# Performance work log

Measured on AMD Instinct MI355X. Metric: run time of the kernel, lower is better.

Reference implementation:

```python
import jax, jax.numpy as jnp
import numpy as np

B, S, F, H = 64, 1024, 128, 512  # batch, seq_len, features, lstm units


def setup_inputs() -> dict:
    key = jax.random.key(0)
    k1, k2, k3 = jax.random.split(key, 3)
    x = jax.random.normal(k1, (B, S, F), dtype=jnp.float32)
    # Keras LSTM params: kernel [F, 4H], recurrent_kernel [H, 4H], bias [4H]
    W = jax.random.normal(k2, (F, 4 * H), dtype=jnp.float32) * (1.0 / np.sqrt(F))
    U = jax.random.normal(k3, (H, 4 * H), dtype=jnp.float32) * (1.0 / np.sqrt(H))
    b = jnp.zeros((4 * H,), dtype=jnp.float32)
    return {"x": x, "W": W, "U": U, "b": b}


def _lstm_relu(x, W, U, b):
    # Precompute input projection for all timesteps: [B,S,4H]
    xW = jnp.einsum("bsf,fg->bsg", x, W) + b
    xW_t = jnp.transpose(xW, (1, 0, 2))  # [S,B,4H] for scan over time
    h0 = jnp.zeros((x.shape[0], H), dtype=x.dtype)
    c0 = jnp.zeros((x.shape[0], H), dtype=x.dtype)

    def step(carry, xw):
        h, c = carry
        z = xw + h @ U  # [B,4H]
        zi, zf, zg, zo = jnp.split(z, 4, axis=-1)  # Keras gate order i,f,c,o
        i = jax.nn.sigmoid(zi)
        f = jax.nn.sigmoid(zf)
        g = jax.nn.relu(zg)          # activation='relu' (candidate)
        o = jax.nn.sigmoid(zo)
        c_new = f * c + i * g
        h_new = o * jax.nn.relu(c_new)  # activation='relu' (output)
        return (h_new, c_new), h_new

    _, hs = jax.lax.scan(step, (h0, c0), xW_t)
    return jnp.transpose(hs, (1, 0, 2))  # [B,S,H]


def reference(x, W, U, b):
    # LSTM(return_sequences=True, activation='relu'); Dropout inactive at inference.
    return _lstm_relu(x, W, U, b)
```

## Files before the change

### kernel.cpp

```cpp
#include <hip/hip_runtime.h>
#include <stdint.h>


#define S_ 1024
#define F_ 128
#define H_ 512
#define G4_ 2048
#define SLOTS 32
#define KH 16
#define LDKS 640
#define HB (64 * H_)

typedef __attribute__((ext_vector_type(8))) short short8;
typedef __attribute__((ext_vector_type(4))) float f32x4;
typedef unsigned long long ull;

__device__ __forceinline__ unsigned short f2bf(float f) {
  union { float f; unsigned u; } v; v.f = f;
  unsigned u = v.u + 0x7fffu + ((v.u >> 16) & 1u);
  return (unsigned short)(u >> 16);
}

__device__ __forceinline__ short8 pack2(f32x4 a, f32x4 b) {
  short8 r;
#pragma unroll
  for (int i = 0; i < 4; ++i) r[i] = (short)f2bf(a[i]);
#pragma unroll
  for (int i = 0; i < 4; ++i) r[4 + i] = (short)f2bf(b[i]);
  return r;
}

__device__ __forceinline__ int swz(int cc, int k) {
  return (cc * LDKS + k) ^ ((cc & 7) << 3);
}

__global__ __launch_bounds__(256, 1) void lstm_pers(
    const float* __restrict__ x, const float* __restrict__ W,
    const float* __restrict__ U, const float* __restrict__ bias,
    float* __restrict__ out, unsigned int* ws_sync, unsigned short* hbuf) {

  __shared__ unsigned short V[64 * LDKS];
  __shared__ f32x4 R[2][4][4][64];
  __shared__ int meta[2];

  const int tid  = threadIdx.x;
  const int w    = tid >> 6;
  const int lane = tid & 63;
  const int l15  = lane & 15;
  const int l4   = lane >> 4;
  const int koff = l4 * 8;

  if (tid == 0) {
    unsigned int xcc;
    asm volatile("s_getreg_b32 %0, hwreg(20, 0, 4)" : "=s"(xcc));
    xcc &= 7;
    unsigned sv = atomicAdd(ws_sync + xcc * 32, 1u);
    meta[0] = (int)xcc;
    meta[1] = (int)(sv & 31);
  }
  __syncthreads();
  const int xcc  = meta[0];
  const int slot = meta[1];

  unsigned int* gflags = ws_sync + 256 + xcc * 128;
  unsigned int* myflag = gflags + slot * 4 + w;
  unsigned int* pollp  = gflags + 32 * w + (lane & 31);

  const int u0    = slot * 16;
  const int bbase = xcc * 8;

  for (int idx = tid; idx < (64 * LDKS) / 4; idx += 256) {
    const int q4   = idx & 15;
    const int k    = idx >> 4;
    const int gate = q4 & 3;
    const int ul0  = (q4 >> 2) * 4;
    const int col  = gate * H_ + u0 + ul0;
    const float* src = (k < H_) ? (U + (size_t)k * G4_ + col)
                                : (W + (size_t)(k - H_) * G4_ + col);
    const f32x4 v4 = *(const f32x4*)src;
#pragma unroll
    for (int q = 0; q < 4; ++q) {
      const int ul = ul0 + q;
      const int cc = (ul >> 2) * 16 + (ul & 3) * 4 + gate;
      V[swz(cc, k)] = f2bf(v4[q]);
    }
  }

  float bias_r[4];
#pragma unroll
  for (int g = 0; g < 4; ++g) bias_r[g] = bias[g * H_ + u0 + w * 4 + l4];

  __syncthreads();

  const int brow = bbase + (l15 & 7);
  const float* xrow = x + (size_t)brow * S_ * F_ + koff + w * 32;
  const unsigned short* hrow0 = hbuf + (size_t)brow * H_ + koff;
  const int myunit = u0 + w * 4 + l4;

  float cst = 0.f;

  f32x4 xa = *(const f32x4*)(xrow);
  f32x4 xb = *(const f32x4*)(xrow + 4);

  for (int t = 0; t < S_; ++t) {
    f32x4 acc[4];
#pragma unroll
    for (int tl = 0; tl < 4; ++tl) { acc[tl][0]=0.f; acc[tl][1]=0.f; acc[tl][2]=0.f; acc[tl][3]=0.f; }
    {
      const short8 bx = pack2(xa, xb);
      const int k0 = (KH + w) * 32 + koff;
#pragma unroll
      for (int tl = 0; tl < 4; ++tl) {
        const short8 a = *(const short8*)&V[swz(tl * 16 + l15, k0)];
        acc[tl] = __builtin_amdgcn_mfma_f32_16x16x32_bf16(a, bx, acc[tl], 0, 0, 0);
      }
    }

    {
      const int tn = (t + 1 < S_) ? t + 1 : t;
      const float* xt = xrow + (size_t)tn * F_;
      xa = *(const f32x4*)(xt);
      xb = *(const f32x4*)(xt + 4);
    }

    if (t > 0) {
      const unsigned tgt = (unsigned)t;
      while (true) {
        unsigned v = __hip_atomic_load(pollp, __ATOMIC_RELAXED, __HIP_MEMORY_SCOPE_AGENT);
        if (__all((int)(v >= tgt))) break;
      }
      asm volatile("" ::: "memory");

      const unsigned short* hr = hrow0 + (size_t)(t & 1) * HB;
      short8 bh[4];
#pragma unroll
      for (int i = 0; i < 4; ++i) {
        union { ull u[2]; short8 s; } bb;
        const ull* hq = (const ull*)(hr + (4 * w + i) * 32);
        bb.u[0] = __hip_atomic_load(hq,     __ATOMIC_RELAXED, __HIP_MEMORY_SCOPE_AGENT);
        bb.u[1] = __hip_atomic_load(hq + 1, __ATOMIC_RELAXED, __HIP_MEMORY_SCOPE_AGENT);
        bh[i] = bb.s;
      }
#pragma unroll
      for (int i = 0; i < 4; ++i) {
        const int k0 = (4 * w + i) * 32 + koff;
#pragma unroll
        for (int tl = 0; tl < 4; ++tl) {
          const short8 a = *(const short8*)&V[swz(tl * 16 + l15, k0)];
          acc[tl] = __builtin_amdgcn_mfma_f32_16x16x32_bf16(a, bh[i], acc[tl], 0, 0, 0);
        }
      }
    }

    const int p = t & 1;
#pragma unroll
    for (int tl = 0; tl < 4; ++tl) R[p][w][tl][lane] = acc[tl];
    __syncthreads();

    f32x4 z;
    {
      const f32x4 r0 = R[p][0][w][lane], r1 = R[p][1][w][lane],
                  r2 = R[p][2][w][lane], r3 = R[p][3][w][lane];
#pragma unroll
      for (int g = 0; g < 4; ++g)
        z[g] = bias_r[g] + r0[g] + r1[g] + r2[g] + r3[g];
    }

    const float ig = 1.f / (1.f + __expf(-z[0]));
    const float fg = 1.f / (1.f + __expf(-z[1]));
    const float gg = fmaxf(z[2], 0.f);
    const float og = 1.f / (1.f + __expf(-z[3]));
    const float cn = fg * cst + ig * gg;
    cst = cn;
    const float hv = og * fmaxf(cn, 0.f);

    if (l15 < 8)
      hbuf[(size_t)((t + 1) & 1) * HB + (size_t)brow * H_ + myunit] = f2bf(hv);
    asm volatile("s_waitcnt vmcnt(0)" ::: "memory");
    if (lane == 0)
      __hip_atomic_store(myflag, (unsigned)(t + 1), __ATOMIC_RELAXED, __HIP_MEMORY_SCOPE_AGENT);
    if (l15 < 8)
      out[((size_t)brow * S_ + t) * H_ + myunit] = hv;
  }
}

extern "C" void kernel_launch(void* const* d_in, const int* in_sizes, int n_in,
                              void* d_out, int out_size, void* d_ws, size_t ws_size,
                              hipStream_t stream) {
  const float* x = (const float*)d_in[0];
  const float* W = (const float*)d_in[1];
  const float* U = (const float*)d_in[2];
  const float* b = (const float*)d_in[3];
  float* out = (float*)d_out;

  unsigned int*   ws_sync = (unsigned int*)d_ws;
  unsigned short* hbuf    = (unsigned short*)((char*)d_ws + 32768);

  hipMemsetAsync(d_ws, 0, 32768, stream);

  lstm_pers<<<dim3(256), dim3(256), 0, stream>>>(x, W, U, b, out, ws_sync, hbuf);
}
```

Measured before the change: 2.732 ms.

## Give each wave its own unit rows and drop the per-step cross-wave reduction

Result: slower. 8.160 ms (+198.7%).

```diff
diff --git a/kernel.cpp b/kernel.cpp
--- a/kernel.cpp
+++ b/kernel.cpp
@@ -6,7 +6,6 @@
 #define F_ 128
 #define H_ 512
 #define G4_ 2048
-#define SLOTS 32
 #define KH 16
 #define LDKS 640
 #define HB (64 * H_)
@@ -40,8 +39,8 @@
     float* __restrict__ out, unsigned int* ws_sync, unsigned short* hbuf) {
 
   __shared__ unsigned short V[64 * LDKS];
-  __shared__ f32x4 R[2][4][4][64];
   __shared__ int meta[2];
+  __shared__ unsigned join_ctr;
 
   const int tid  = threadIdx.x;
   const int w    = tid >> 6;
@@ -57,14 +56,13 @@
     unsigned sv = atomicAdd(ws_sync + xcc * 32, 1u);
     meta[0] = (int)xcc;
     meta[1] = (int)(sv & 31);
+    join_ctr = 0u;
   }
   __syncthreads();
   const int xcc  = meta[0];
   const int slot = meta[1];
 
-  unsigned int* gflags = ws_sync + 256 + xcc * 128;
-  unsigned int* myflag = gflags + slot * 4 + w;
-  unsigned int* pollp  = gflags + 32 * w + (lane & 31);
+  unsigned int* gline = ws_sync + 256 + xcc * 32;
 
   const int u0    = slot * 16;
   const int bbase = xcc * 8;
@@ -93,78 +91,73 @@
   __syncthreads();
 
   const int brow = bbase + (l15 & 7);
-  const float* xrow = x + (size_t)brow * S_ * F_ + koff + w * 32;
+  const float* xrow = x + (size_t)brow * S_ * F_ + koff;
   const unsigned short* hrow0 = hbuf + (size_t)brow * H_ + koff;
   const int myunit = u0 + w * 4 + l4;
+  const int vrow   = w * 16 + l15;
 
   float cst = 0.f;
 
-  f32x4 xa = *(const f32x4*)(xrow);
-  f32x4 xb = *(const f32x4*)(xrow + 4);
+  f32x4 xa[4], xb[4];
+#pragma unroll
+  for (int q = 0; q < 4; ++q) {
+    xa[q] = *(const f32x4*)(xrow + q * 32);
+    xb[q] = *(const f32x4*)(xrow + q * 32 + 4);
+  }
 
   for (int t = 0; t < S_; ++t) {
     f32x4 acc[4];
 #pragma unroll
-    for (int tl = 0; tl < 4; ++tl) { acc[tl][0]=0.f; acc[tl][1]=0.f; acc[tl][2]=0.f; acc[tl][3]=0.f; }
-    {
-      const short8 bx = pack2(xa, xb);
-      const int k0 = (KH + w) * 32 + koff;
-#pragma unroll
-      for (int tl = 0; tl < 4; ++tl) {
-        const short8 a = *(const short8*)&V[swz(tl * 16 + l15, k0)];
-        acc[tl] = __builtin_amdgcn_mfma_f32_16x16x32_bf16(a, bx, acc[tl], 0, 0, 0);
-      }
+    for (int q = 0; q < 4; ++q) { acc[q][0]=0.f; acc[q][1]=0.f; acc[q][2]=0.f; acc[q][3]=0.f; }
+
+#pragma unroll
+    for (int q = 0; q < 4; ++q) {
+      const short8 bx = pack2(xa[q], xb[q]);
+      const short8 a  = *(const short8*)&V[swz(vrow, (KH + q) * 32 + koff)];
+      acc[q] = __builtin_amdgcn_mfma_f32_16x16x32_bf16(a, bx, acc[q], 0, 0, 0);
     }
 
     {
       const int tn = (t + 1 < S_) ? t + 1 : t;
       const float* xt = xrow + (size_t)tn * F_;
-      xa = *(const f32x4*)(xt);
-      xb = *(const f32x4*)(xt + 4);
+#pragma unroll
+      for (int q = 0; q < 4; ++q) {
+        xa[q] = *(const f32x4*)(xt + q * 32);
+        xb[q] = *(const f32x4*)(xt + q * 32 + 4);
+      }
     }
 
     if (t > 0) {
       const unsigned tgt = (unsigned)t;
-      while (true) {
-        unsigned v = __hip_atomic_load(pollp, __ATOMIC_RELAXED, __HIP_MEMORY_SCOPE_AGENT);
-        if (__all((int)(v >= tgt))) break;
-      }
-      asm volatile("" ::: "memory");
-
       const unsigned short* hr = hrow0 + (size_t)(t & 1) * HB;
-      short8 bh[4];
-#pragma unroll
-      for (int i = 0; i < 4; ++i) {
-        union { ull u[2]; short8 s; } bb;
-        const ull* hq = (const ull*)(hr + (4 * w + i) * 32);
-        bb.u[0] = __hip_atomic_load(hq,     __ATOMIC_RELAXED, __HIP_MEMORY_SCOPE_AGENT);
-        bb.u[1] = __hip_atomic_load(hq + 1, __ATOMIC_RELAXED, __HIP_MEMORY_SCOPE_AGENT);
-        bh[i] = bb.s;
-      }
-#pragma unroll
-      for (int i = 0; i < 4; ++i) {
-        const int k0 = (4 * w + i) * 32 + koff;
-#pragma unroll
-        for (int tl = 0; tl < 4; ++tl) {
-          const short8 a = *(const short8*)&V[swz(tl * 16 + l15, k0)];
-          acc[tl] = __builtin_amdgcn_mfma_f32_16x16x32_bf16(a, bh[i], acc[tl], 0, 0, 0);
+#pragma unroll
+      for (int ci = 0; ci < 4; ++ci) {
+        const int c = (w + ci) & 3;
+        while (true) {
+          const unsigned fl = __hip_atomic_load(gline + (lane & 31),
+                                                __ATOMIC_RELAXED, __HIP_MEMORY_SCOPE_AGENT);
+          ull m = __ballot((int)(fl >= tgt));
+          m &= (m >> 32);
+          if (((m >> (8 * c)) & 0xFFull) == 0xFFull) break;
+        }
+        asm volatile("" ::: "memory");
+#pragma unroll
+        for (int i = 0; i < 4; ++i) {
+          const int ks = 4 * c + i;
+          union { ull u[2]; short8 s; } bb;
+          const ull* hq = (const ull*)(hr + ks * 32);
+          bb.u[0] = __hip_atomic_load(hq,     __ATOMIC_RELAXED, __HIP_MEMORY_SCOPE_AGENT);
+          bb.u[1] = __hip_atomic_load(hq + 1, __ATOMIC_RELAXED, __HIP_MEMORY_SCOPE_AGENT);
+          const short8 a = *(const short8*)&V[swz(vrow, ks * 32 + koff)];
+          acc[ci] = __builtin_amdgcn_mfma_f32_16x16x32_bf16(a, bb.s, acc[ci], 0, 0, 0);
         }
       }
     }
 
-    const int p = t & 1;
-#pragma unroll
-    for (int tl = 0; tl < 4; ++tl) R[p][w][tl][lane] = acc[tl];
-    __syncthreads();
-
     f32x4 z;
-    {
-      const f32x4 r0 = R[p][0][w][lane], r1 = R[p][1][w][lane],
-                  r2 = R[p][2][w][lane], r3 = R[p][3][w][lane];
-#pragma unroll
-      for (int g = 0; g < 4; ++g)
-        z[g] = bias_r[g] + r0[g] + r1[g] + r2[g] + r3[g];
-    }
+#pragma unroll
+    for (int g = 0; g < 4; ++g)
+      z[g] = bias_r[g] + acc[0][g] + acc[1][g] + acc[2][g] + acc[3][g];
 
     const float ig = 1.f / (1.f + __expf(-z[0]));
     const float fg = 1.f / (1.f + __expf(-z[1]));
@@ -177,8 +170,14 @@
     if (l15 < 8)
       hbuf[(size_t)((t + 1) & 1) * HB + (size_t)brow * H_ + myunit] = f2bf(hv);
     asm volatile("s_waitcnt vmcnt(0)" ::: "memory");
-    if (lane == 0)
-      __hip_atomic_store(myflag, (unsigned)(t + 1), __ATOMIC_RELAXED, __HIP_MEMORY_SCOPE_AGENT);
+
+    if (lane == 0) {
+      const unsigned old = atomicAdd(&join_ctr, 1u);
+      if (old == 4u * (unsigned)t + 3u)
+        __hip_atomic_store(gline + slot, (unsigned)(t + 1),
+                           __ATOMIC_RELAXED, __HIP_MEMORY_SCOPE_AGENT);
+    }
+
     if (l15 < 8)
       out[((size_t)brow * S_ + t) * H_ + myunit] = hv;
   }
```

## Embed parity flags in h sign bits and replace swizzle with LDS padding

Applied to the files above, without the earlier changes.

After: 2.716 ms. Within noise of the previous version (-0.6%).

```diff
diff --git a/kernel.cpp b/kernel.cpp
--- a/kernel.cpp
+++ b/kernel.cpp
@@ -6,10 +6,12 @@
 #define F_ 128
 #define H_ 512
 #define G4_ 2048
-#define SLOTS 32
 #define KH 16
-#define LDKS 640
+#define KDIM 640
+#define LDKS 648
 #define HB (64 * H_)
+#define SMASK 0x8000800080008000ull
+#define VMASK 0x7FFF7FFF7FFF7FFFull
 
 typedef __attribute__((ext_vector_type(8))) short short8;
 typedef __attribute__((ext_vector_type(4))) float f32x4;
@@ -28,10 +30,6 @@
 #pragma unroll
   for (int i = 0; i < 4; ++i) r[4 + i] = (short)f2bf(b[i]);
   return r;
-}
-
-__device__ __forceinline__ int swz(int cc, int k) {
-  return (cc * LDKS + k) ^ ((cc & 7) << 3);
 }
 
 __global__ __launch_bounds__(256, 1) void lstm_pers(
@@ -62,14 +60,14 @@
   const int xcc  = meta[0];
   const int slot = meta[1];
 
-  unsigned int* gflags = ws_sync + 256 + xcc * 128;
-  unsigned int* myflag = gflags + slot * 4 + w;
-  unsigned int* pollp  = gflags + 32 * w + (lane & 31);
+  unsigned int* eline = ws_sync + 256 + xcc * 32;
+  unsigned int* myep  = eline + slot;
+  unsigned int* epp   = eline + (lane & 31);
 
   const int u0    = slot * 16;
   const int bbase = xcc * 8;
 
-  for (int idx = tid; idx < (64 * LDKS) / 4; idx += 256) {
+  for (int idx = tid; idx < (64 * KDIM) / 4; idx += 256) {
     const int q4   = idx & 15;
     const int k    = idx >> 4;
     const int gate = q4 & 3;
@@ -82,7 +80,7 @@
     for (int q = 0; q < 4; ++q) {
       const int ul = ul0 + q;
       const int cc = (ul >> 2) * 16 + (ul & 3) * 4 + gate;
-      V[swz(cc, k)] = f2bf(v4[q]);
+      V[cc * LDKS + k] = f2bf(v4[q]);
     }
   }
 
@@ -103,6 +101,10 @@
   f32x4 xb = *(const f32x4*)(xrow + 4);
 
   for (int t = 0; t < S_; ++t) {
+    unsigned ev = 0xFFFFFFFFu;
+    if (w == 0 && t >= 2)
+      ev = __hip_atomic_load(epp, __ATOMIC_RELAXED, __HIP_MEMORY_SCOPE_AGENT);
+
     f32x4 acc[4];
 #pragma unroll
     for (int tl = 0; tl < 4; ++tl) { acc[tl][0]=0.f; acc[tl][1]=0.f; acc[tl][2]=0.f; acc[tl][3]=0.f; }
@@ -111,7 +113,7 @@
       const int k0 = (KH + w) * 32 + koff;
 #pragma unroll
       for (int tl = 0; tl < 4; ++tl) {
-        const short8 a = *(const short8*)&V[swz(tl * 16 + l15, k0)];
+        const short8 a = *(const short8*)&V[(tl * 16 + l15) * LDKS + k0];
         acc[tl] = __builtin_amdgcn_mfma_f32_16x16x32_bf16(a, bx, acc[tl], 0, 0, 0);
       }
     }
@@ -124,29 +126,40 @@
     }
 
     if (t > 0) {
-      const unsigned tgt = (unsigned)t;
+      const ull expm = (((((t - 1) >> 1) & 1) ^ 1) ? SMASK : 0ull);
+      const unsigned short* hr = hrow0 + (size_t)(t & 1) * HB;
+      const ull* q0 = (const ull*)(hr + (4 * w + 0) * 32);
+      const ull* q1 = (const ull*)(hr + (4 * w + 1) * 32);
+      const ull* q2 = (const ull*)(hr + (4 * w + 2) * 32);
+      const ull* q3 = (const ull*)(hr + (4 * w + 3) * 32);
+      ull v0, v1, v2, v3, v4, v5, v6, v7;
       while (true) {
-        unsigned v = __hip_atomic_load(pollp, __ATOMIC_RELAXED, __HIP_MEMORY_SCOPE_AGENT);
-        if (__all((int)(v >= tgt))) break;
+        v0 = __hip_atomic_load(q0,     __ATOMIC_RELAXED, __HIP_MEMORY_SCOPE_AGENT);
+        v1 = __hip_atomic_load(q0 + 1, __ATOMIC_RELAXED, __HIP_MEMORY_SCOPE_AGENT);
+        v2 = __hip_atomic_load(q1,     __ATOMIC_RELAXED, __HIP_MEMORY_SCOPE_AGENT);
+        v3 = __hip_atomic_load(q1 + 1, __ATOMIC_RELAXED, __HIP_MEMORY_SCOPE_AGENT);
+        v4 = __hip_atomic_load(q2,     __ATOMIC_RELAXED, __HIP_MEMORY_SCOPE_AGENT);
+        v5 = __hip_atomic_load(q2 + 1, __ATOMIC_RELAXED, __HIP_MEMORY_SCOPE_AGENT);
+        v6 = __hip_atomic_load(q3,     __ATOMIC_RELAXED, __HIP_MEMORY_SCOPE_AGENT);
+        v7 = __hip_atomic_load(q3 + 1, __ATOMIC_RELAXED, __HIP_MEMORY_SCOPE_AGENT);
+        const bool ok = ((v0 & SMASK) == expm) & ((v1 & SMASK) == expm) &
+                        ((v2 & SMASK) == expm) & ((v3 & SMASK) == expm) &
+                        ((v4 & SMASK) == expm) & ((v5 & SMASK) == expm) &
+                        ((v6 & SMASK) == expm) & ((v7 & SMASK) == expm);
+        if (__all((int)ok)) break;
       }
-      asm volatile("" ::: "memory");
-
-      const unsigned short* hr = hrow0 + (size_t)(t & 1) * HB;
-      short8 bh[4];
-#pragma unroll
-      for (int i = 0; i < 4; ++i) {
-        union { ull u[2]; short8 s; } bb;
-        const ull* hq = (const ull*)(hr + (4 * w + i) * 32);
-        bb.u[0] = __hip_atomic_load(hq,     __ATOMIC_RELAXED, __HIP_MEMORY_SCOPE_AGENT);
-        bb.u[1] = __hip_atomic_load(hq + 1, __ATOMIC_RELAXED, __HIP_MEMORY_SCOPE_AGENT);
-        bh[i] = bb.s;
-      }
+      union { ull u[2]; short8 s; } b0, b1, b2, b3;
+      b0.u[0] = v0 & VMASK; b0.u[1] = v1 & VMASK;
+      b1.u[0] = v2 & VMASK; b1.u[1] = v3 & VMASK;
+      b2.u[0] = v4 & VMASK; b2.u[1] = v5 & VMASK;
+      b3.u[0] = v6 & VMASK; b3.u[1] = v7 & VMASK;
+      const short8 bh[4] = {b0.s, b1.s, b2.s, b3.s};
 #pragma unroll
       for (int i = 0; i < 4; ++i) {
         const int k0 = (4 * w + i) * 32 + koff;
 #pragma unroll
         for (int tl = 0; tl < 4; ++tl) {
-          const short8 a = *(const short8*)&V[swz(tl * 16 + l15, k0)];
+          const short8 a = *(const short8*)&V[(tl * 16 + l15) * LDKS + k0];
           acc[tl] = __builtin_amdgcn_mfma_f32_16x16x32_bf16(a, bh[i], acc[tl], 0, 0, 0);
         }
       }
@@ -155,7 +168,16 @@
     const int p = t & 1;
 #pragma unroll
     for (int tl = 0; tl < 4; ++tl) R[p][w][tl][lane] = acc[tl];
+
+    if (w == 0 && t >= 2) {
+      const unsigned tgt = (unsigned)(t - 1);
+      while (!__all((int)(ev >= tgt)))
+        ev = __hip_atomic_load(epp, __ATOMIC_RELAXED, __HIP_MEMORY_SCOPE_AGENT);
+    }
     __syncthreads();
+
+    if (w == 1 && lane == 0)
+      __hip_atomic_store(myep, (unsigned)t, __ATOMIC_RELAXED, __HIP_MEMORY_SCOPE_AGENT);
 
     f32x4 z;
     {
@@ -174,13 +196,14 @@
     cst = cn;
     const float hv = og * fmaxf(cn, 0.f);
 
-    if (l15 < 8)
-      hbuf[(size_t)((t + 1) & 1) * HB + (size_t)brow * H_ + myunit] = f2bf(hv);
-    asm volatile("s_waitcnt vmcnt(0)" ::: "memory");
-    if (lane == 0)
-      __hip_atomic_store(myflag, (unsigned)(t + 1), __ATOMIC_RELAXED, __HIP_MEMORY_SCOPE_AGENT);
-    if (l15 < 8)
+    if (l15 < 8) {
+      const unsigned short sm =
+          (unsigned short)(((((unsigned)t >> 1) & 1u) ^ 1u) << 15);
+      __hip_atomic_store(&hbuf[(size_t)((t + 1) & 1) * HB + (size_t)brow * H_ + myunit],
+                         (unsigned short)(f2bf(hv) | sm),
+                         __ATOMIC_RELAXED, __HIP_MEMORY_SCOPE_AGENT);
       out[((size_t)brow * S_ + t) * H_ + myunit] = hv;
+    }
   }
 }
 
@@ -196,7 +219,7 @@
   unsigned int*   ws_sync = (unsigned int*)d_ws;
   unsigned short* hbuf    = (unsigned short*)((char*)d_ws + 32768);
 
-  hipMemsetAsync(d_ws, 0, 32768, stream);
+  hipMemsetAsync(d_ws, 0, 32768 + 2 * HB * sizeof(unsigned short), stream);
 
   lstm_pers<<<dim3(256), dim3(256), 0, stream>>>(x, W, U, b, out, ws_sync, hbuf);
 }
```
